# Kernel tuning notes

Measured on AMD Instinct MI355X. Metric: run time of the kernel, lower is better.

Reference implementation:

```python
import jax, jax.numpy as jnp
import numpy as np
import math

N_HEAD = 16
N_EMBD = 1024


def setup_inputs() -> dict:
    key = jax.random.key(0)
    ks = jax.random.split(key, 8)
    B, T, C = 2, 2048, N_EMBD
    x = jax.random.normal(ks[0], (B, T, C), dtype=jnp.float32)
    # Linear weights stored as [in, out] (transposed vs torch's [out, in])
    W_attn = jax.random.normal(ks[1], (C, 3 * C), dtype=jnp.float32) * (1.0 / math.sqrt(C))
    b_attn = jnp.zeros((3 * C,), dtype=jnp.float32)
    W_proj = jax.random.normal(ks[2], (C, C), dtype=jnp.float32) * (1.0 / math.sqrt(C))
    b_proj = jnp.zeros((C,), dtype=jnp.float32)
    threshold = jnp.full((N_HEAD,), 0.01, dtype=jnp.float32)
    leak = jnp.full((N_HEAD,), 2.0, dtype=jnp.float32)
    steepness = jnp.full((N_HEAD,), 2.0, dtype=jnp.float32)
    return {"x": x, "W_attn": W_attn, "b_attn": b_attn, "W_proj": W_proj,
            "b_proj": b_proj, "threshold": threshold, "leak": leak,
            "steepness": steepness}


def reference(x, W_attn, b_attn, W_proj, b_proj, threshold, leak, steepness):
    B, T, C = x.shape
    H = N_HEAD
    hd = C // H
    qkv = x @ W_attn + b_attn  # [B, T, 3C]
    q, k, v = jnp.split(qkv, 3, axis=-1)
    # [B, H, T, hd]
    q = q.reshape(B, T, H, hd).transpose(0, 2, 1, 3)
    k = k.reshape(B, T, H, hd).transpose(0, 2, 1, 3)
    v = v.reshape(B, T, H, hd).transpose(0, 2, 1, 3)

    att = jnp.einsum('bhqd,bhkd->bhqk', q, k) * (1.0 / math.sqrt(hd))
    causal = jnp.tril(jnp.ones((T, T), dtype=bool))  # [T, T]
    att = jnp.where(causal[None, None, :, :], att, -jnp.inf)

    probs = jax.nn.softmax(att, axis=-1)  # [B, H, T, T]
    thr = (jnp.abs(threshold) * 0.1).reshape(1, H, 1, 1)
    lk = jax.nn.sigmoid(leak).reshape(1, H, 1, 1)
    st = jax.nn.softplus(steepness).reshape(1, H, 1, 1)
    fire = jax.nn.sigmoid(st * (probs - thr))
    lif_w = fire + lk * (1.0 - fire)
    mod = probs * lif_w
    mod = mod / (jnp.sum(mod, axis=-1, keepdims=True) + 1e-8)

    y = jnp.einsum('bhqk,bhkd->bhqd', mod, v)  # [B, H, T, hd]
    y = y.transpose(0, 2, 1, 3).reshape(B, T, C)
    return y @ W_proj + b_proj
```

## Files before the change

kernel.cpp:

```cpp
#include <hip/hip_runtime.h>
#include <hip/hip_bf16.h>
#include <math.h>

#define NHEAD 16
#define HD 64
#define TSEQ 2048
#define CEMB 1024

typedef __attribute__((ext_vector_type(8))) short short8;
typedef __attribute__((ext_vector_type(4))) float f32x4;
typedef __attribute__((ext_vector_type(16))) float f32x16;

__device__ inline unsigned short f2bf(float f) {
  union { float f; unsigned u; } x; x.f = f;
  unsigned r = x.u + 0x7FFFu + ((x.u >> 16) & 1u);
  return (unsigned short)(r >> 16);
}

__device__ inline unsigned pk2(float a, float b) {
  __hip_bfloat162 t = __float22bfloat162_rn(make_float2(a, b));
  union { __hip_bfloat162 v; unsigned u; } c; c.v = t;
  return c.u;
}

__device__ inline float ex2(float x) {
#if __has_builtin(__builtin_amdgcn_exp2f)
  return __builtin_amdgcn_exp2f(x);
#else
  float r; asm("v_exp_f32 %0, %1" : "=v"(r) : "v"(x)); return r;
#endif
}

__device__ inline void gload16(const void* g, void* l) {
  __builtin_amdgcn_global_load_lds(
      (const __attribute__((address_space(1))) unsigned int*)g,
      (__attribute__((address_space(3))) unsigned int*)l, 16, 0, 0);
}

__global__ __launch_bounds__(256) void castx(const float* __restrict__ in,
                                             unsigned short* __restrict__ out) {
  int i = blockIdx.x * 256 + threadIdx.x;
  float4 v = ((const float4*)in)[i];
  ushort4 o;
  o.x = f2bf(v.x); o.y = f2bf(v.y); o.z = f2bf(v.z); o.w = f2bf(v.w);
  ((ushort4*)out)[i] = o;
}

__global__ __launch_bounds__(256) void transW(const float* __restrict__ W,
                                              unsigned short* __restrict__ Wt,
                                              int N) {
  __shared__ float t[64][65];
  const int tid = threadIdx.x;
  const int rb = blockIdx.y * 64;
  const int cb = blockIdx.x * 64;
#pragma unroll
  for (int i = 0; i < 16; ++i) {
    int idx = i * 256 + tid, r = idx >> 6, cl = idx & 63;
    t[r][cl] = W[(size_t)(rb + r) * N + cb + cl];
  }
  __syncthreads();
#pragma unroll
  for (int i = 0; i < 16; ++i) {
    int idx = i * 256 + tid, r = idx >> 6, cl = idx & 63;
    Wt[(size_t)(cb + r) * 1024 + rb + cl] = f2bf(t[cl][r]);
  }
}

template <int MODE>
__global__ __launch_bounds__(256) void mm128(const unsigned short* __restrict__ A,
                                             const unsigned short* __restrict__ Bt,
                                             const float* __restrict__ bias,
                                             void* __restrict__ out0,
                                             unsigned short* __restrict__ ko,
                                             unsigned short* __restrict__ vto) {
  __shared__ __align__(16) unsigned char Asm[16384];
  __shared__ __align__(16) unsigned char Bsm[16384];
  const int tid = threadIdx.x;
  const int lane = tid & 63;
  const int w = tid >> 6;
  const int wm = w >> 1, wn = w & 1;
  const int c = lane & 15, g = lane >> 4;
  const int rowbase = blockIdx.y * 128;
  const int colbase = blockIdx.x * 128;

  f32x4 acc[4][4];
#pragma unroll
  for (int m = 0; m < 4; ++m)
#pragma unroll
    for (int n = 0; n < 4; ++n) acc[m][n] = (f32x4){0.f, 0.f, 0.f, 0.f};

  const unsigned char* Ab = (const unsigned char*)(A + (size_t)rowbase * 1024);
  const unsigned char* Bb = (const unsigned char*)(Bt + (size_t)colbase * 1024);
  const int swz = (c & 7) << 4;

  for (int kt = 0; kt < 16; ++kt) {
    __syncthreads();
#pragma unroll
    for (int it = 0; it < 4; ++it) {
      const int L = it * 4096 + tid * 16;
      const int row = L >> 7;
      const int sc = (L & 127) ^ ((row & 7) << 4);
      gload16(Ab + (size_t)row * 2048 + kt * 128 + sc, Asm + L);
      gload16(Bb + (size_t)row * 2048 + kt * 128 + sc, Bsm + L);
    }
    __syncthreads();
#pragma unroll
    for (int ks = 0; ks < 2; ++ks) {
      const int cb = ks * 64 + 16 * g;
      short8 af[4], bf[4];
#pragma unroll
      for (int m = 0; m < 4; ++m)
        af[m] = *(const short8*)(Asm + (wm * 64 + m * 16 + c) * 128 + (cb ^ swz));
#pragma unroll
      for (int n = 0; n < 4; ++n)
        bf[n] = *(const short8*)(Bsm + (wn * 64 + n * 16 + c) * 128 + (cb ^ swz));
#pragma unroll
      for (int m = 0; m < 4; ++m)
#pragma unroll
        for (int n = 0; n < 4; ++n)
          acc[m][n] = __builtin_amdgcn_mfma_f32_16x16x32_bf16(af[m], bf[n], acc[m][n], 0, 0, 0);
    }
  }

#pragma unroll
  for (int m = 0; m < 4; ++m) {
    const int rw = rowbase + wm * 64 + m * 16 + 4 * g;
#pragma unroll
    for (int n = 0; n < 4; ++n) {
      const int col = colbase + wn * 64 + n * 16 + c;
      const float bz = bias[col];
      if (MODE == 0) {
        unsigned short* qo = (unsigned short*)out0;
        const int sel = col >> 10, cc = col & 1023, hh = cc >> 6, d = cc & 63;
#pragma unroll
        for (int r = 0; r < 4; ++r) {
          const int row = rw + r;
          const int b = row >> 11, t = row & 2047;
          const float val = acc[m][n][r] + bz;
          const size_t bh = (size_t)(b * NHEAD + hh);
          if (sel == 0)
            qo[(bh * TSEQ + t) * HD + d] = f2bf(val * 0.18033688011112042f);
          else if (sel == 1)
            ko[(bh * TSEQ + t) * HD + d] = f2bf(val);
          else
            vto[(bh * HD + d) * TSEQ + t] = f2bf(val);
        }
      } else {
        float* out = (float*)out0;
#pragma unroll
        for (int r = 0; r < 4; ++r)
          out[(size_t)(rw + r) * 1024 + col] = acc[m][n][r] + bz;
      }
    }
  }
}

__global__ __launch_bounds__(256) void lif_sw(
    const unsigned short* __restrict__ qb,
    const unsigned short* __restrict__ kb,
    const unsigned short* __restrict__ vtb,
    const float* __restrict__ thr_p, const float* __restrict__ leak_p,
    const float* __restrict__ steep_p,
    unsigned short* __restrict__ y) {
  __shared__ float obuf[4][32][33];
  __shared__ float lbufA[4][32];
  __shared__ float lbufB[4][32];
  __shared__ float msbuf[4][32];

  const int bh = blockIdx.x;
  const int h = bh & (NHEAD - 1);
  const int b = bh >> 4;
  const int tid = threadIdx.x;
  const int s = tid >> 6;
  const int lane = tid & 63;
  const int qv = lane & 31;
  const int hi = lane >> 5;
  const int klb = 4 * hi;

  const int qtA = 63 - blockIdx.y;
  const int qtB = blockIdx.y;
  const int ntA = qtA + 1, ntB = qtB + 1;
  const int nt4a = (ntA + 3) >> 2;
  const int t0a = s * nt4a;
  const int t1a = min(t0a + nt4a, ntA);

  const unsigned short* qp = qb + (size_t)bh * TSEQ * HD;
  const unsigned short* kp = kb + (size_t)bh * TSEQ * HD;
  const unsigned short* vp = vtb + (size_t)bh * HD * TSEQ;

  const float thr = fabsf(thr_p[h]) * 0.1f;
  const float lk = 1.f / (1.f + __expf(-leak_p[h]));
  const float st = log1pf(__expf(steep_p[h]));
  const float stc = st * 1.44269504088896f;
  const float stthr2 = stc * thr;
  const float omlk = 1.f - lk;

  const unsigned short* kpl  = kp + (size_t)qv * HD + 8 * hi;
  const unsigned short* vpl0 = vp + (size_t)qv * TSEQ + 8 * hi;
  const unsigned short* vpl1 = vp + (size_t)(32 + qv) * TSEQ + 8 * hi;

  const unsigned short* qplA = qp + (size_t)(qtA * 32 + qv) * HD + 8 * hi;
  const short8 qfA0 = *(const short8*)(qplA);
  const short8 qfA1 = *(const short8*)(qplA + 16);
  const short8 qfA2 = *(const short8*)(qplA + 32);
  const short8 qfA3 = *(const short8*)(qplA + 48);
  const unsigned short* qplB = qp + (size_t)(qtB * 32 + qv) * HD + 8 * hi;
  const short8 qfB0 = *(const short8*)(qplB);
  const short8 qfB1 = *(const short8*)(qplB + 16);
  const short8 qfB2 = *(const short8*)(qplB + 32);
  const short8 qfB3 = *(const short8*)(qplB + 48);

  float lA = 0.f, lB = 0.f;
  for (int t = t0a; t < t1a; ++t) {
    const unsigned short* kt = kpl + (size_t)t * (32 * HD);
    const short8 k0 = *(const short8*)(kt);
    const short8 k1 = *(const short8*)(kt + 16);
    const short8 k2 = *(const short8*)(kt + 32);
    const short8 k3 = *(const short8*)(kt + 48);
    f32x16 sa = {};
    sa = __builtin_amdgcn_mfma_f32_32x32x16_bf16(k0, qfA0, sa, 0, 0, 0);
    sa = __builtin_amdgcn_mfma_f32_32x32x16_bf16(k1, qfA1, sa, 0, 0, 0);
    sa = __builtin_amdgcn_mfma_f32_32x32x16_bf16(k2, qfA2, sa, 0, 0, 0);
    sa = __builtin_amdgcn_mfma_f32_32x32x16_bf16(k3, qfA3, sa, 0, 0, 0);
    if (t == qtA) {
#pragma unroll
      for (int j = 0; j < 16; ++j)
        if ((j & 3) + 8 * (j >> 2) + klb > qv) sa[j] = -1e30f;
    }
#pragma unroll
    for (int j = 0; j < 16; ++j) lA += ex2(sa[j]);
    if (t < ntB) {
      f32x16 sb = {};
      sb = __builtin_amdgcn_mfma_f32_32x32x16_bf16(k0, qfB0, sb, 0, 0, 0);
      sb = __builtin_amdgcn_mfma_f32_32x32x16_bf16(k1, qfB1, sb, 0, 0, 0);
      sb = __builtin_amdgcn_mfma_f32_32x32x16_bf16(k2, qfB2, sb, 0, 0, 0);
      sb = __builtin_amdgcn_mfma_f32_32x32x16_bf16(k3, qfB3, sb, 0, 0, 0);
      if (t == qtB) {
#pragma unroll
        for (int j = 0; j < 16; ++j)
          if ((j & 3) + 8 * (j >> 2) + klb > qv) sb[j] = -1e30f;
      }
#pragma unroll
      for (int j = 0; j < 16; ++j) lB += ex2(sb[j]);
    }
  }
  lA += __shfl_xor(lA, 32, 64);
  lB += __shfl_xor(lB, 32, 64);
  if (hi == 0) { lbufA[s][qv] = lA; lbufB[s][qv] = lB; }
  __syncthreads();
  const float stli2A =
      stc / ((lbufA[0][qv] + lbufA[1][qv]) + (lbufA[2][qv] + lbufA[3][qv]));
  const float stli2B =
      stc / ((lbufB[0][qv] + lbufB[1][qv]) + (lbufB[2][qv] + lbufB[3][qv]));

  f32x16 o0, o1;
  float ms;
  auto passB = [&](int t0, int t1, int qt, float stli2, const short8& q0,
                   const short8& q1, const short8& q2, const short8& q3) {
    o0 = (f32x16){}; o1 = (f32x16){};
    ms = 0.f;
    for (int t = t0; t < t1; ++t) {
      const unsigned short* kt = kpl + (size_t)t * (32 * HD);
      f32x16 sv = {};
      sv = __builtin_amdgcn_mfma_f32_32x32x16_bf16(*(const short8*)(kt), q0, sv, 0, 0, 0);
      sv = __builtin_amdgcn_mfma_f32_32x32x16_bf16(*(const short8*)(kt + 16), q1, sv, 0, 0, 0);
      sv = __builtin_amdgcn_mfma_f32_32x32x16_bf16(*(const short8*)(kt + 32), q2, sv, 0, 0, 0);
      sv = __builtin_amdgcn_mfma_f32_32x32x16_bf16(*(const short8*)(kt + 48), q3, sv, 0, 0, 0);
      const unsigned short* v0 = vpl0 + t * 32;
      const unsigned short* v1 = vpl1 + t * 32;
      short8 va00 = *(const short8*)(v0);
      short8 va01 = *(const short8*)(v0 + 16);
      short8 va10 = *(const short8*)(v1);
      short8 va11 = *(const short8*)(v1 + 16);

      if (t == qt) {
#pragma unroll
        for (int j = 0; j < 16; ++j)
          if ((j & 3) + 8 * (j >> 2) + klb > qv) sv[j] = -1e30f;
      }
      unsigned cw[8];
#pragma unroll
      for (int jj = 0; jj < 8; ++jj) {
        float e0 = ex2(sv[2 * jj]);
        float e1 = ex2(sv[2 * jj + 1]);
        float u0 = ex2(fmaf(-stli2, e0, stthr2));
        float u1 = ex2(fmaf(-stli2, e1, stthr2));
        float f0 = __builtin_amdgcn_rcpf(1.f + u0);
        float f1 = __builtin_amdgcn_rcpf(1.f + u1);
        float m0 = e0 * fmaf(omlk, f0, lk);
        float m1 = e1 * fmaf(omlk, f1, lk);
        ms += m0;
        ms += m1;
        cw[jj] = pk2(m0, m1);
      }
      asm("v_permlane32_swap_b32 %0, %1" : "+v"(cw[0]), "+v"(cw[2]));
      asm("v_permlane32_swap_b32 %0, %1" : "+v"(cw[1]), "+v"(cw[3]));
      asm("v_permlane32_swap_b32 %0, %1" : "+v"(cw[4]), "+v"(cw[6]));
      asm("v_permlane32_swap_b32 %0, %1" : "+v"(cw[5]), "+v"(cw[7]));
      union { unsigned u[4]; short8 v; } B0, B1;
      B0.u[0] = cw[0]; B0.u[1] = cw[1]; B0.u[2] = cw[2]; B0.u[3] = cw[3];
      B1.u[0] = cw[4]; B1.u[1] = cw[5]; B1.u[2] = cw[6]; B1.u[3] = cw[7];

      o0 = __builtin_amdgcn_mfma_f32_32x32x16_bf16(va00, B0.v, o0, 0, 0, 0);
      o0 = __builtin_amdgcn_mfma_f32_32x32x16_bf16(va01, B1.v, o0, 0, 0, 0);
      o1 = __builtin_amdgcn_mfma_f32_32x32x16_bf16(va10, B0.v, o1, 0, 0, 0);
      o1 = __builtin_amdgcn_mfma_f32_32x32x16_bf16(va11, B1.v, o1, 0, 0, 0);
    }
  };

  auto writeout = [&](int qbase) {
    ms += __shfl_xor(ms, 32, 64);
    if (hi == 0) msbuf[s][qv] = ms;
#pragma unroll
    for (int j = 0; j < 16; ++j) {
      const int dl = (j & 3) + 8 * (j >> 2) + klb;
      obuf[s][qv][dl] = o0[j];
    }
    __syncthreads();
    {
      const int dl = tid & 31;
      const int qq = tid >> 5;
#pragma unroll
      for (int it = 0; it < 4; ++it) {
        const int q = qq * 4 + it;
        const float acc = (obuf[0][q][dl] + obuf[1][q][dl]) +
                          (obuf[2][q][dl] + obuf[3][q][dl]);
        const float mt = (msbuf[0][q] + msbuf[1][q]) + (msbuf[2][q] + msbuf[3][q]);
        y[((size_t)(b * TSEQ) + qbase + q) * CEMB + h * HD + dl] =
            f2bf(acc / (mt + 1e-8f));
      }
    }
    __syncthreads();
#pragma unroll
    for (int j = 0; j < 16; ++j) {
      const int dl = (j & 3) + 8 * (j >> 2) + klb;
      obuf[s][qv][dl] = o1[j];
    }
    __syncthreads();
    {
      const int dl = tid & 31;
      const int qq = tid >> 5;
#pragma unroll
      for (int it = 0; it < 4; ++it) {
        const int q = qq * 4 + it;
        const float acc = (obuf[0][q][dl] + obuf[1][q][dl]) +
                          (obuf[2][q][dl] + obuf[3][q][dl]);
        const float mt = (msbuf[0][q] + msbuf[1][q]) + (msbuf[2][q] + msbuf[3][q]);
        y[((size_t)(b * TSEQ) + qbase + q) * CEMB + h * HD + 32 + dl] =
            f2bf(acc / (mt + 1e-8f));
      }
    }
    __syncthreads();
  };

  passB(t0a, t1a, qtA, stli2A, qfA0, qfA1, qfA2, qfA3);
  writeout(qtA * 32);

  const int nt4b = (ntB + 3) >> 2;
  const int t0b = s * nt4b;
  const int t1b = min(t0b + nt4b, ntB);
  passB(t0b, t1b, qtB, stli2B, qfB0, qfB1, qfB2, qfB3);
  writeout(qtB * 32);
}

extern "C" void kernel_launch(void* const* d_in, const int* in_sizes, int n_in,
                              void* d_out, int out_size, void* d_ws, size_t ws_size,
                              hipStream_t stream) {
  const float* x      = (const float*)d_in[0];
  const float* W_attn = (const float*)d_in[1];
  const float* b_attn = (const float*)d_in[2];
  const float* W_proj = (const float*)d_in[3];
  const float* b_proj = (const float*)d_in[4];
  const float* thr    = (const float*)d_in[5];
  const float* leak   = (const float*)d_in[6];
  const float* steep  = (const float*)d_in[7];
  float* out = (float*)d_out;

  unsigned short* xb   = (unsigned short*)d_ws;
  unsigned short* Wat  = xb + (size_t)4096 * 1024;
  unsigned short* Wpt  = Wat + (size_t)3072 * 1024;
  unsigned short* qws  = Wpt + (size_t)1024 * 1024;
  unsigned short* kws  = qws + (size_t)32 * 2048 * 64;
  unsigned short* vtws = kws + (size_t)32 * 2048 * 64;
  unsigned short* yb   = vtws + (size_t)32 * 2048 * 64;

  castx<<<4096, 256, 0, stream>>>(x, xb);
  transW<<<dim3(48, 16), 256, 0, stream>>>(W_attn, Wat, 3072);
  transW<<<dim3(16, 16), 256, 0, stream>>>(W_proj, Wpt, 1024);
  mm128<0><<<dim3(24, 32), 256, 0, stream>>>(xb, Wat, b_attn, qws, kws, vtws);
  lif_sw<<<dim3(32, 32), 256, 0, stream>>>(qws, kws, vtws, thr, leak, steep, yb);
  mm128<1><<<dim3(8, 32), 256, 0, stream>>>(yb, Wpt, b_proj, out, nullptr, nullptr);
}
```

Baseline: 186.9 us.

## Interleave key tiles across waves and merge output reduction into one pass

```diff
diff --git a/kernel.cpp b/kernel.cpp
--- a/kernel.cpp
+++ b/kernel.cpp
@@ -162,7 +162,7 @@
     const float* __restrict__ thr_p, const float* __restrict__ leak_p,
     const float* __restrict__ steep_p,
     unsigned short* __restrict__ y) {
-  __shared__ float obuf[4][32][33];
+  __shared__ float obuf[8][32][33];
   __shared__ float lbufA[4][32];
   __shared__ float lbufB[4][32];
   __shared__ float msbuf[4][32];
@@ -180,9 +180,6 @@
   const int qtA = 63 - blockIdx.y;
   const int qtB = blockIdx.y;
   const int ntA = qtA + 1, ntB = qtB + 1;
-  const int nt4a = (ntA + 3) >> 2;
-  const int t0a = s * nt4a;
-  const int t1a = min(t0a + nt4a, ntA);
 
   const unsigned short* qp = qb + (size_t)bh * TSEQ * HD;
   const unsigned short* kp = kb + (size_t)bh * TSEQ * HD;
@@ -211,30 +208,33 @@
   const short8 qfB3 = *(const short8*)(qplB + 48);
 
   float lA = 0.f, lB = 0.f;
-  for (int t = t0a; t < t1a; ++t) {
+  for (int t = s; t < ntA; t += 4) {
     const unsigned short* kt = kpl + (size_t)t * (32 * HD);
     const short8 k0 = *(const short8*)(kt);
     const short8 k1 = *(const short8*)(kt + 16);
     const short8 k2 = *(const short8*)(kt + 32);
     const short8 k3 = *(const short8*)(kt + 48);
+    const bool doB = (t < ntB);
     f32x16 sa = {};
     sa = __builtin_amdgcn_mfma_f32_32x32x16_bf16(k0, qfA0, sa, 0, 0, 0);
     sa = __builtin_amdgcn_mfma_f32_32x32x16_bf16(k1, qfA1, sa, 0, 0, 0);
     sa = __builtin_amdgcn_mfma_f32_32x32x16_bf16(k2, qfA2, sa, 0, 0, 0);
     sa = __builtin_amdgcn_mfma_f32_32x32x16_bf16(k3, qfA3, sa, 0, 0, 0);
-    if (t == qtA) {
-#pragma unroll
-      for (int j = 0; j < 16; ++j)
-        if ((j & 3) + 8 * (j >> 2) + klb > qv) sa[j] = -1e30f;
-    }
-#pragma unroll
-    for (int j = 0; j < 16; ++j) lA += ex2(sa[j]);
-    if (t < ntB) {
-      f32x16 sb = {};
+    f32x16 sb = {};
+    if (doB) {
       sb = __builtin_amdgcn_mfma_f32_32x32x16_bf16(k0, qfB0, sb, 0, 0, 0);
       sb = __builtin_amdgcn_mfma_f32_32x32x16_bf16(k1, qfB1, sb, 0, 0, 0);
       sb = __builtin_amdgcn_mfma_f32_32x32x16_bf16(k2, qfB2, sb, 0, 0, 0);
       sb = __builtin_amdgcn_mfma_f32_32x32x16_bf16(k3, qfB3, sb, 0, 0, 0);
+    }
+    if (t == qtA) {
+#pragma unroll
+      for (int j = 0; j < 16; ++j)
+        if ((j & 3) + 8 * (j >> 2) + klb > qv) sa[j] = -1e30f;
+    }
+#pragma unroll
+    for (int j = 0; j < 16; ++j) lA += ex2(sa[j]);
+    if (doB) {
       if (t == qtB) {
 #pragma unroll
         for (int j = 0; j < 16; ++j)
@@ -255,11 +255,11 @@
 
   f32x16 o0, o1;
   float ms;
-  auto passB = [&](int t0, int t1, int qt, float stli2, const short8& q0,
+  auto passB = [&](int nt, int qt, float stli2, const short8& q0,
                    const short8& q1, const short8& q2, const short8& q3) {
     o0 = (f32x16){}; o1 = (f32x16){};
     ms = 0.f;
-    for (int t = t0; t < t1; ++t) {
+    for (int t = s; t < nt; t += 4) {
       const unsigned short* kt = kpl + (size_t)t * (32 * HD);
       f32x16 sv = {};
       sv = __builtin_amdgcn_mfma_f32_32x32x16_bf16(*(const short8*)(kt), q0, sv, 0, 0, 0);
@@ -300,7 +300,6 @@
       union { unsigned u[4]; short8 v; } B0, B1;
       B0.u[0] = cw[0]; B0.u[1] = cw[1]; B0.u[2] = cw[2]; B0.u[3] = cw[3];
       B1.u[0] = cw[4]; B1.u[1] = cw[5]; B1.u[2] = cw[6]; B1.u[3] = cw[7];
-
       o0 = __builtin_amdgcn_mfma_f32_32x32x16_bf16(va00, B0.v, o0, 0, 0, 0);
       o0 = __builtin_amdgcn_mfma_f32_32x32x16_bf16(va01, B1.v, o0, 0, 0, 0);
       o1 = __builtin_amdgcn_mfma_f32_32x32x16_bf16(va10, B0.v, o1, 0, 0, 0);
@@ -314,52 +313,29 @@
 #pragma unroll
     for (int j = 0; j < 16; ++j) {
       const int dl = (j & 3) + 8 * (j >> 2) + klb;
-      obuf[s][qv][dl] = o0[j];
+      obuf[s * 2 + 0][qv][dl] = o0[j];
+      obuf[s * 2 + 1][qv][dl] = o1[j];
     }
     __syncthreads();
     {
-      const int dl = tid & 31;
-      const int qq = tid >> 5;
-#pragma unroll
-      for (int it = 0; it < 4; ++it) {
-        const int q = qq * 4 + it;
-        const float acc = (obuf[0][q][dl] + obuf[1][q][dl]) +
-                          (obuf[2][q][dl] + obuf[3][q][dl]);
+      const int d = tid & 63;
+      const int db = d >> 5, dl = d & 31;
+#pragma unroll
+      for (int it = 0; it < 8; ++it) {
+        const int q = (tid >> 6) * 8 + it;
+        const float acc = ((obuf[0 + db][q][dl] + obuf[2 + db][q][dl]) +
+                           (obuf[4 + db][q][dl] + obuf[6 + db][q][dl]));
         const float mt = (msbuf[0][q] + msbuf[1][q]) + (msbuf[2][q] + msbuf[3][q]);
-        y[((size_t)(b * TSEQ) + qbase + q) * CEMB + h * HD + dl] =
-            f2bf(acc / (mt + 1e-8f));
-      }
-    }
-    __syncthreads();
-#pragma unroll
-    for (int j = 0; j < 16; ++j) {
-      const int dl = (j & 3) + 8 * (j >> 2) + klb;
-      obuf[s][qv][dl] = o1[j];
-    }
-    __syncthreads();
-    {
-      const int dl = tid & 31;
-      const int qq = tid >> 5;
-#pragma unroll
-      for (int it = 0; it < 4; ++it) {
-        const int q = qq * 4 + it;
-        const float acc = (obuf[0][q][dl] + obuf[1][q][dl]) +
-                          (obuf[2][q][dl] + obuf[3][q][dl]);
-        const float mt = (msbuf[0][q] + msbuf[1][q]) + (msbuf[2][q] + msbuf[3][q]);
-        y[((size_t)(b * TSEQ) + qbase + q) * CEMB + h * HD + 32 + dl] =
+        y[((size_t)(b * TSEQ) + qbase + q) * CEMB + h * HD + d] =
             f2bf(acc / (mt + 1e-8f));
       }
     }
     __syncthreads();
   };
 
-  passB(t0a, t1a, qtA, stli2A, qfA0, qfA1, qfA2, qfA3);
+  passB(ntA, qtA, stli2A, qfA0, qfA1, qfA2, qfA3);
   writeout(qtA * 32);
-
-  const int nt4b = (ntB + 3) >> 2;
-  const int t0b = s * nt4b;
-  const int t1b = min(t0b + nt4b, ntB);
-  passB(t0b, t1b, qtB, stli2B, qfB0, qfB1, qfB2, qfB3);
+  passB(ntB, qtB, stli2B, qfB0, qfB1, qfB2, qfB3);
   writeout(qtB * 32);
 }
 
```

After: 186.0 us. About the same (-0.5%).
